# Optimization experiments

Measured on AMD Instinct MI355X. Metric: run time of the kernel, lower is better.

## Reference

```python
import jax, jax.numpy as jnp
import numpy as np

N, E, IN, HID, HEADS, L = 50000, 640000, 32, 64, 2, 4
MAXR = 8
N_ETYPE = 11 + 3 * MAXR  # 35
NEG_SLOPE = 0.2  # DGL EGATConv leaky_relu slope


def _mlp2(x, W1, b1, W2, b2):
    # 2-layer MLP: activation (gelu) after hidden layer only
    return jax.nn.gelu(x @ W1 + b1) @ W2 + b2


def _egat(h, ef, src, dst, W_ni, W_nj, W_fij, W_node, b_node, attn):
    # DGL EGATConv: edge-feature-enhanced graph attention
    n = h.shape[0]
    H, D = attn.shape
    f_edge = (h @ W_ni)[src] + (h @ W_nj)[dst] + ef @ W_fij       # [E, H*D]
    f_out = jax.nn.leaky_relu(f_edge, NEG_SLOPE).reshape(-1, H, D)
    e = jnp.einsum('ehd,hd->eh', f_out, attn)                     # [E, H]
    m = jax.ops.segment_max(e, dst, num_segments=n)               # per-dst max
    w = jnp.exp(e - m[dst])
    z = jax.ops.segment_sum(w, dst, num_segments=n)
    a = w / z[dst]                                                # edge softmax over incoming edges
    h_out = (h @ W_node + b_node).reshape(n, H, D)
    return jax.ops.segment_sum(h_out[src] * a[:, :, None], dst, num_segments=n)  # [N, H, D]


def _forward(feat, att_rc, att_rp, type_emb, rid_emb, rc_W, rc_b, rp_W, rp_b,
             fe_W1, fe_b1, fe_W2, fe_b2, W_ni, W_nj, W_fij, W_node, b_node, attn,
             mlp_W1, mlp_b1, mlp_W2, mlp_b2, src, dst, etype, erid):
    n = feat.shape[0]
    # edge embedding, 'sum' flavor
    ef = type_emb[etype] + rid_emb[erid] + att_rc @ rc_W + rc_b + att_rp @ rp_W + rp_b
    feats = [feat]
    h = _mlp2(feat, fe_W1, fe_b1, fe_W2, fe_b2)
    feats.append(h)
    for l in range(W_ni.shape[0]):
        agg = _egat(h, ef, src, dst, W_ni[l], W_nj[l], W_fij[l],
                    W_node[l], b_node[l], attn[l])
        h = _mlp2(agg.reshape(n, -1), mlp_W1[l], mlp_b1[l], mlp_W2[l], mlp_b2[l]) + h  # residual
        feats.append(h)
    node_emb = jnp.concatenate(feats, axis=-1)             # layer_pooling='all'
    graph_emb = jnp.max(node_emb, axis=0, keepdims=True)   # graph max pooling
    return jnp.concatenate([node_emb, jnp.broadcast_to(graph_emb, node_emb.shape)], axis=-1)


def setup_inputs() -> dict:
    key = jax.random.key(0)
    ks = iter(jax.random.split(key, 40))
    s = 0.05
    return {
        'feat': jax.random.normal(next(ks), (N, IN), jnp.float32),
        'att_rc': jax.random.normal(next(ks), (E, 2), jnp.float32),
        'att_rp': jax.random.normal(next(ks), (E, 3), jnp.float32),
        'type_emb': jax.random.normal(next(ks), (N_ETYPE, HID), jnp.float32) * s,
        'rid_emb': jax.random.normal(next(ks), (MAXR + 1, HID), jnp.float32) * s,
        'rc_W': jax.random.normal(next(ks), (2, HID), jnp.float32) * s,
        'rc_b': jnp.zeros((HID,), jnp.float32),
        'rp_W': jax.random.normal(next(ks), (3, HID), jnp.float32) * s,
        'rp_b': jnp.zeros((HID,), jnp.float32),
        'fe_W1': jax.random.normal(next(ks), (IN, HID), jnp.float32) * s,
        'fe_b1': jnp.zeros((HID,), jnp.float32),
        'fe_W2': jax.random.normal(next(ks), (HID, HID), jnp.float32) * s,
        'fe_b2': jnp.zeros((HID,), jnp.float32),
        'W_ni': jax.random.normal(next(ks), (L, HID, HEADS * HID), jnp.float32) * s,
        'W_nj': jax.random.normal(next(ks), (L, HID, HEADS * HID), jnp.float32) * s,
        'W_fij': jax.random.normal(next(ks), (L, HID, HEADS * HID), jnp.float32) * s,
        'W_node': jax.random.normal(next(ks), (L, HID, HEADS * HID), jnp.float32) * s,
        'b_node': jnp.zeros((L, HEADS * HID), jnp.float32),
        'attn': jax.random.normal(next(ks), (L, HEADS, HID), jnp.float32) * s,
        'mlp_W1': jax.random.normal(next(ks), (L, HEADS * HID, HEADS * HID), jnp.float32) * s,
        'mlp_b1': jnp.zeros((L, HEADS * HID), jnp.float32),
        'mlp_W2': jax.random.normal(next(ks), (L, HEADS * HID, HID), jnp.float32) * s,
        'mlp_b2': jnp.zeros((L, HID), jnp.float32),
        'src': jax.random.randint(next(ks), (E,), 0, N, jnp.int32),
        'dst': jax.random.randint(next(ks), (E,), 0, N, jnp.int32),
        'etype': jax.random.randint(next(ks), (E,), 0, N_ETYPE, jnp.int32),
        'erid': jax.random.randint(next(ks), (E,), 0, MAXR + 1, jnp.int32),
    }


def reference(feat, att_rc, att_rp, type_emb, rid_emb, rc_W, rc_b, rp_W, rp_b,
              fe_W1, fe_b1, fe_W2, fe_b2, W_ni, W_nj, W_fij, W_node, b_node, attn,
              mlp_W1, mlp_b1, mlp_W2, mlp_b2, src, dst, etype, erid):
    return _forward(feat, att_rc, att_rp, type_emb, rid_emb, rc_W, rc_b, rp_W, rp_b,
                    fe_W1, fe_b1, fe_W2, fe_b2, W_ni, W_nj, W_fij, W_node, b_node, attn,
                    mlp_W1, mlp_b1, mlp_W2, mlp_b2, src, dst, etype, erid)
```

## Files before the change

### kernel.cpp

```cpp
#include <hip/hip_runtime.h>
#include <math.h>

#define N_NODES 50000
#define N_EDGES 640000
#define NLAYER  4
#define NPAD    50016

typedef unsigned short bf16_t;
typedef __attribute__((ext_vector_type(8))) short s16x8;
typedef __attribute__((ext_vector_type(4))) float f32x4;

__device__ __forceinline__ float gelu_f(float x) {
    return 0.5f * x * (1.0f + tanhf(0.7978845608028654f * (x + 0.044715f * x * x * x)));
}

__device__ __forceinline__ bf16_t f2bf(float f) {
    unsigned u = __float_as_uint(f);
    unsigned r = (u + 0x7FFFu + ((u >> 16) & 1u)) >> 16;
    return (bf16_t)r;
}
__device__ __forceinline__ float bf2f(bf16_t h) { return __uint_as_float(((unsigned)h) << 16); }
__device__ __forceinline__ float bfl(unsigned x) { return __uint_as_float(x << 16); }
__device__ __forceinline__ float bfh(unsigned x) { return __uint_as_float(x & 0xFFFF0000u); }

__global__ void k_zero32(unsigned* p, int n) {
    int i = blockIdx.x * 256 + threadIdx.x;
    if (i < n) p[i] = 0u;
}

__global__ void k_hist(const int* __restrict__ dst, int* __restrict__ deg) {
    int i = blockIdx.x * 256 + threadIdx.x;
    if (i < N_EDGES) atomicAdd(&deg[dst[i]], 1);
}

__global__ void k_scan1(const int* __restrict__ deg, int* __restrict__ rowptr, int* __restrict__ bsum) {
    __shared__ int sd[1024];
    int gi = blockIdx.x * 1024 + threadIdx.x;
    int v = (gi < N_NODES) ? deg[gi] : 0;
    sd[threadIdx.x] = v;
    __syncthreads();
    for (int off = 1; off < 1024; off <<= 1) {
        int t2 = (threadIdx.x >= (unsigned)off) ? sd[threadIdx.x - off] : 0;
        __syncthreads();
        sd[threadIdx.x] += t2;
        __syncthreads();
    }
    if (gi < N_NODES) rowptr[gi] = sd[threadIdx.x] - v;
    if (threadIdx.x == 1023) bsum[blockIdx.x] = sd[1023];
}

__global__ void k_scan2(const int* __restrict__ bsum, int* __restrict__ boff, int nb) {
    if (threadIdx.x == 0 && blockIdx.x == 0) {
        int run = 0;
        for (int b = 0; b < nb; b++) { boff[b] = run; run += bsum[b]; }
    }
}

__global__ void k_scan3(int* __restrict__ rowptr, const int* __restrict__ boff) {
    int gi = blockIdx.x * 1024 + threadIdx.x;
    if (gi < N_NODES) rowptr[gi] += boff[blockIdx.x];
    if (gi == 0) rowptr[N_NODES] = N_EDGES;
}

__global__ void k_copy(const int* __restrict__ a, int* __restrict__ b) {
    int i = blockIdx.x * 256 + threadIdx.x;
    if (i < N_NODES) b[i] = a[i];
}

__global__ void k_scatter(const int* __restrict__ dst, int* __restrict__ cursor, int* __restrict__ eidx) {
    int i = blockIdx.x * 256 + threadIdx.x;
    if (i < N_EDGES) {
        int p = atomicAdd(&cursor[dst[i]], 1);
        eidx[p] = i;
    }
}

__global__ void k_sortgather(
    const int* __restrict__ eidx, const int* __restrict__ src, const int* __restrict__ dst,
    const int* __restrict__ etype, const int* __restrict__ erid,
    const float* __restrict__ att_rc, const float* __restrict__ att_rp,
    int* __restrict__ src_s, uint4* __restrict__ emA, uint2* __restrict__ emB)
{
    int i = blockIdx.x * 256 + threadIdx.x;
    if (i < N_EDGES) {
        int e = eidx[i];
        int sv = src[e];
        src_s[i] = sv;
        uint4 a;
        a.x = (unsigned)sv;
        a.y = (unsigned)dst[e];
        a.z = (unsigned)(etype[e] * 9 + erid[e]);
        a.w = (unsigned)f2bf(att_rc[2 * e]) | ((unsigned)f2bf(att_rc[2 * e + 1]) << 16);
        uint2 b;
        b.x = (unsigned)f2bf(att_rp[3 * e]) | ((unsigned)f2bf(att_rp[3 * e + 1]) << 16);
        b.y = (unsigned)f2bf(att_rp[3 * e + 2]);
        emA[i] = a;
        emB[i] = b;
    }
}

__global__ void k_base(const float* __restrict__ type_emb, const float* __restrict__ rid_emb,
                       const float* __restrict__ rcb, const float* __restrict__ rpb,
                       float* __restrict__ base)
{
    int idx = blockIdx.x * 256 + threadIdx.x;
    if (idx >= 315 * 64) return;
    int c = idx >> 6, k = idx & 63;
    int et = c / 9, er = c % 9;
    base[idx] = type_emb[et * 64 + k] + rid_emb[er * 64 + k] + rcb[k] + rpb[k];
}

__global__ void k_wprep(const float* __restrict__ Wfij, const float* __restrict__ Wni,
                        const float* __restrict__ Wnj, const float* __restrict__ Wnode,
                        const float* __restrict__ W1, const float* __restrict__ W2,
                        bf16_t* __restrict__ WT, bf16_t* __restrict__ W3T,
                        bf16_t* __restrict__ W1T, bf16_t* __restrict__ W2T)
{
    int idx = blockIdx.x * 256 + threadIdx.x;
    if (idx >= NLAYER * 57344) return;
    int l = idx / 57344, r = idx % 57344;
    if (r < 8192) {
        int n = r >> 6, k = r & 63;
        WT[l * 8192 + r] = f2bf(Wfij[l * 8192 + k * 128 + n]);
    } else if (r < 32768) {
        int q = r - 8192; int c = q >> 6, k = q & 63;
        const float* src = (c < 128) ? Wni : (c < 256) ? Wnj : Wnode;
        W3T[l * 24576 + q] = f2bf(src[l * 8192 + k * 128 + (c & 127)]);
    } else if (r < 49152) {
        int q = r - 32768; int n = q >> 7, k = q & 127;
        W1T[l * 16384 + q] = f2bf(W1[l * 16384 + k * 128 + n]);
    } else {
        int q = r - 49152; int j = q >> 7, k = q & 127;
        W2T[l * 8192 + q] = f2bf(W2[l * 8192 + k * 64 + j]);
    }
}

__global__ __launch_bounds__(256) void k_fe(
    const float* __restrict__ feat, const float* __restrict__ W1, const float* __restrict__ b1,
    const float* __restrict__ W2, const float* __restrict__ b2,
    float* __restrict__ h, bf16_t* __restrict__ hb, float* __restrict__ out)
{
    __shared__ float hid[4][64];
    int w = threadIdx.x >> 6, lane = threadIdx.x & 63;
    int n = blockIdx.x * 4 + w;
    float a = b1[lane];
#pragma unroll 8
    for (int k = 0; k < 32; k++) a = fmaf(feat[n * 32 + k], W1[k * 64 + lane], a);
    hid[w][lane] = gelu_f(a);
    __syncthreads();
    float o = b2[lane];
#pragma unroll 8
    for (int k = 0; k < 64; k++) o = fmaf(hid[w][k], W2[k * 64 + lane], o);
    h[n * 64 + lane] = o;
    hb[n * 64 + lane] = f2bf(o);
    out[n * 704 + 32 + lane] = o;
    if (lane < 32) out[n * 704 + lane] = feat[n * 32 + lane];
}

__global__ __launch_bounds__(256) void k_node3(
    const bf16_t* __restrict__ hb, const bf16_t* __restrict__ W3T,
    const float* __restrict__ bnode, bf16_t* __restrict__ s)
{
    __shared__ __align__(16) bf16_t hbS[32 * 72];
    const int t = threadIdx.x;
    const int wave = t >> 6, lane = t & 63, l16 = lane & 15, quad = lane >> 4;
    const int n0 = blockIdx.x * 32;
    {
        int r = t >> 3, sg = t & 7;
        *(s16x8*)(hbS + r * 72 + sg * 8) = *(const s16x8*)(hb + (size_t)(n0 + r) * 64 + sg * 8);
    }
    __syncthreads();
    const int ng = wave & 1, ch = wave >> 1;
    const s16x8 B0 = *(const s16x8*)(hbS + (ng * 16 + l16) * 72 + quad * 8);
    const s16x8 B1 = *(const s16x8*)(hbS + (ng * 16 + l16) * 72 + 32 + quad * 8);
    const int node = n0 + ng * 16 + l16;
#pragma unroll
    for (int nt = 0; nt < 12; nt++) {
        int c0 = ch * 192 + nt * 16;
        const s16x8 A0 = *(const s16x8*)(W3T + (size_t)(c0 + l16) * 64 + quad * 8);
        const s16x8 A1 = *(const s16x8*)(W3T + (size_t)(c0 + l16) * 64 + 32 + quad * 8);
        f32x4 acc = {0.f, 0.f, 0.f, 0.f};
        acc = __builtin_amdgcn_mfma_f32_16x16x32_bf16(A0, B0, acc, 0, 0, 0);
        acc = __builtin_amdgcn_mfma_f32_16x16x32_bf16(A1, B1, acc, 0, 0, 0);
        int cb = c0 + quad * 4;
        float4 bv = make_float4(0.f, 0.f, 0.f, 0.f);
        if (cb >= 256) bv = *(const float4*)(bnode + cb - 256);
        ushort4 o;
        o.x = f2bf(acc[0] + bv.x);
        o.y = f2bf(acc[1] + bv.y);
        o.z = f2bf(acc[2] + bv.z);
        o.w = f2bf(acc[3] + bv.w);
        *(ushort4*)(s + (size_t)node * 384 + cb) = o;
    }
}

__global__ __launch_bounds__(256) void k_edge(
    const bf16_t* __restrict__ s, const bf16_t* __restrict__ WT,
    const float* __restrict__ attn, const uint4* __restrict__ emA,
    const uint2* __restrict__ emB, const float* __restrict__ base,
    const float* __restrict__ rcW, const float* __restrict__ rpW,
    float* __restrict__ evals)
{
    const int lane = threadIdx.x & 63;
    const int l16 = lane & 15, quad = lane >> 4;
    const int unit = (blockIdx.x * 256 + threadIdx.x) >> 6;
    const int iA = unit * 32 + l16, iB = iA + 16;

    const uint4 mA = emA[iA], mB = emA[iB];
    const uint2 nA = emB[iA], nB = emB[iB];

    ushort4 nivA[4], njvA[4], nivB[4], njvB[4];
    {
        const bf16_t* srA = s + (size_t)mA.x * 384;
        const bf16_t* drA = s + (size_t)mA.y * 384 + 128;
        const bf16_t* srB = s + (size_t)mB.x * 384;
        const bf16_t* drB = s + (size_t)mB.y * 384 + 128;
#pragma unroll
        for (int mt = 0; mt < 4; mt++) {
            const int d0 = mt * 16 + quad * 4;
            nivA[mt] = *(const ushort4*)(srA + d0);
            njvA[mt] = *(const ushort4*)(drA + d0);
            nivB[mt] = *(const ushort4*)(srB + d0);
            njvB[mt] = *(const ushort4*)(drB + d0);
        }
    }

    const float rcA0 = bfl(mA.w), rcA1 = bfh(mA.w);
    const float rpA0 = bfl(nA.x), rpA1 = bfh(nA.x), rpA2 = bfl(nA.y);
    const float rcB0 = bfl(mB.w), rcB1 = bfh(mB.w);
    const float rpB0 = bfl(nB.x), rpB1 = bfh(nB.x), rpB2 = bfl(nB.y);
    const float* bpA = base + (size_t)mA.z * 64;
    const float* bpB = base + (size_t)mB.z * 64;

    s16x8 B0A, B1A, B0B, B1B;
#pragma unroll
    for (int s4 = 0; s4 < 4; s4++) {
        const int k = (s4 >> 1) * 32 + (s4 & 1) * 4 + quad * 8;
        const float4 w0 = *(const float4*)(rcW + k);
        const float4 w1 = *(const float4*)(rcW + 64 + k);
        const float4 w2 = *(const float4*)(rpW + k);
        const float4 w3 = *(const float4*)(rpW + 64 + k);
        const float4 w4 = *(const float4*)(rpW + 128 + k);
        const float4 bA = *(const float4*)(bpA + k);
        const float4 bB = *(const float4*)(bpB + k);
        float a0 = bA.x, a1 = bA.y, a2 = bA.z, a3 = bA.w;
        a0 = fmaf(rcA0, w0.x, a0); a1 = fmaf(rcA0, w0.y, a1); a2 = fmaf(rcA0, w0.z, a2); a3 = fmaf(rcA0, w0.w, a3);
        a0 = fmaf(rcA1, w1.x, a0); a1 = fmaf(rcA1, w1.y, a1); a2 = fmaf(rcA1, w1.z, a2); a3 = fmaf(rcA1, w1.w, a3);
        a0 = fmaf(rpA0, w2.x, a0); a1 = fmaf(rpA0, w2.y, a1); a2 = fmaf(rpA0, w2.z, a2); a3 = fmaf(rpA0, w2.w, a3);
        a0 = fmaf(rpA1, w3.x, a0); a1 = fmaf(rpA1, w3.y, a1); a2 = fmaf(rpA1, w3.z, a2); a3 = fmaf(rpA1, w3.w, a3);
        a0 = fmaf(rpA2, w4.x, a0); a1 = fmaf(rpA2, w4.y, a1); a2 = fmaf(rpA2, w4.z, a2); a3 = fmaf(rpA2, w4.w, a3);
        float b0 = bB.x, b1 = bB.y, b2 = bB.z, b3 = bB.w;
        b0 = fmaf(rcB0, w0.x, b0); b1 = fmaf(rcB0, w0.y, b1); b2 = fmaf(rcB0, w0.z, b2); b3 = fmaf(rcB0, w0.w, b3);
        b0 = fmaf(rcB1, w1.x, b0); b1 = fmaf(rcB1, w1.y, b1); b2 = fmaf(rcB1, w1.z, b2); b3 = fmaf(rcB1, w1.w, b3);
        b0 = fmaf(rpB0, w2.x, b0); b1 = fmaf(rpB0, w2.y, b1); b2 = fmaf(rpB0, w2.z, b2); b3 = fmaf(rpB0, w2.w, b3);
        b0 = fmaf(rpB1, w3.x, b0); b1 = fmaf(rpB1, w3.y, b1); b2 = fmaf(rpB1, w3.z, b2); b3 = fmaf(rpB1, w3.w, b3);
        b0 = fmaf(rpB2, w4.x, b0); b1 = fmaf(rpB2, w4.y, b1); b2 = fmaf(rpB2, w4.z, b2); b3 = fmaf(rpB2, w4.w, b3);
        const short pA0 = (short)f2bf(a0), pA1 = (short)f2bf(a1), pA2 = (short)f2bf(a2), pA3 = (short)f2bf(a3);
        const short pB0 = (short)f2bf(b0), pB1 = (short)f2bf(b1), pB2 = (short)f2bf(b2), pB3 = (short)f2bf(b3);
        const int o = (s4 & 1) * 4;
        if (s4 < 2) {
            B0A[o + 0] = pA0; B0A[o + 1] = pA1; B0A[o + 2] = pA2; B0A[o + 3] = pA3;
            B0B[o + 0] = pB0; B0B[o + 1] = pB1; B0B[o + 2] = pB2; B0B[o + 3] = pB3;
        } else {
            B1A[o + 0] = pA0; B1A[o + 1] = pA1; B1A[o + 2] = pA2; B1A[o + 3] = pA3;
            B1B[o + 0] = pB0; B1B[o + 1] = pB1; B1B[o + 2] = pB2; B1B[o + 3] = pB3;
        }
    }

    float sndA[4][4], sndB[4][4];
#pragma unroll
    for (int mt = 0; mt < 4; mt++) {
        sndA[mt][0] = bf2f(nivA[mt].x) + bf2f(njvA[mt].x);
        sndA[mt][1] = bf2f(nivA[mt].y) + bf2f(njvA[mt].y);
        sndA[mt][2] = bf2f(nivA[mt].z) + bf2f(njvA[mt].z);
        sndA[mt][3] = bf2f(nivA[mt].w) + bf2f(njvA[mt].w);
        sndB[mt][0] = bf2f(nivB[mt].x) + bf2f(njvB[mt].x);
        sndB[mt][1] = bf2f(nivB[mt].y) + bf2f(njvB[mt].y);
        sndB[mt][2] = bf2f(nivB[mt].z) + bf2f(njvB[mt].z);
        sndB[mt][3] = bf2f(nivB[mt].w) + bf2f(njvB[mt].w);
    }

#pragma unroll
    for (int hd = 0; hd < 2; hd++) {
        float pA = 0.f, pB = 0.f;
#pragma unroll
        for (int mt = 0; mt < 4; mt++) {
            const bf16_t* arow = WT + (hd * 64 + mt * 16 + l16) * 64 + quad * 8;
            const s16x8 A0 = *(const s16x8*)(arow);
            const s16x8 A1 = *(const s16x8*)(arow + 32);
            f32x4 aA = {0.f, 0.f, 0.f, 0.f};
            aA = __builtin_amdgcn_mfma_f32_16x16x32_bf16(A0, B0A, aA, 0, 0, 0);
            aA = __builtin_amdgcn_mfma_f32_16x16x32_bf16(A1, B1A, aA, 0, 0, 0);
            f32x4 aB = {0.f, 0.f, 0.f, 0.f};
            aB = __builtin_amdgcn_mfma_f32_16x16x32_bf16(A0, B0B, aB, 0, 0, 0);
            aB = __builtin_amdgcn_mfma_f32_16x16x32_bf16(A1, B1B, aB, 0, 0, 0);
            const float4 at = *(const float4*)(attn + hd * 64 + mt * 16 + quad * 4);
            float f0 = aA[0] + sndA[mt][0];
            float f1 = aA[1] + sndA[mt][1];
            float f2 = aA[2] + sndA[mt][2];
            float f3 = aA[3] + sndA[mt][3];
            f0 = (f0 >= 0.f) ? f0 : 0.2f * f0;
            f1 = (f1 >= 0.f) ? f1 : 0.2f * f1;
            f2 = (f2 >= 0.f) ? f2 : 0.2f * f2;
            f3 = (f3 >= 0.f) ? f3 : 0.2f * f3;
            pA = fmaf(f0, at.x, pA);
            pA = fmaf(f1, at.y, pA);
            pA = fmaf(f2, at.z, pA);
            pA = fmaf(f3, at.w, pA);
            float g0 = aB[0] + sndB[mt][0];
            float g1 = aB[1] + sndB[mt][1];
            float g2 = aB[2] + sndB[mt][2];
            float g3 = aB[3] + sndB[mt][3];
            g0 = (g0 >= 0.f) ? g0 : 0.2f * g0;
            g1 = (g1 >= 0.f) ? g1 : 0.2f * g1;
            g2 = (g2 >= 0.f) ? g2 : 0.2f * g2;
            g3 = (g3 >= 0.f) ? g3 : 0.2f * g3;
            pB = fmaf(g0, at.x, pB);
            pB = fmaf(g1, at.y, pB);
            pB = fmaf(g2, at.z, pB);
            pB = fmaf(g3, at.w, pB);
        }
        pA += __shfl_xor(pA, 16);
        pA += __shfl_xor(pA, 32);
        pB += __shfl_xor(pB, 16);
        pB += __shfl_xor(pB, 32);
        if (quad == 0) {
            evals[iA * 2 + hd] = pA;
            evals[iB * 2 + hd] = pB;
        }
    }
}

__global__ __launch_bounds__(256) void k_soft_agg(
    const int* __restrict__ rowptr, const int* __restrict__ src_s,
    const float* __restrict__ evals, const bf16_t* __restrict__ s,
    unsigned* __restrict__ aggb)
{
    int lane = threadIdx.x & 63;
    int wid = (blockIdx.x * 256 + threadIdx.x) >> 6;
    int nw = (gridDim.x * 256) >> 6;
    const int hb = (lane >> 4) & 1;
    const int esel = lane >> 5;
    const int s32 = (lane & 15) | ((lane >> 5) << 4);
    const int dsel = (lane & 31) * 4;
    for (int n = wid; n < N_NODES; n += nw) {
        int r0 = rowptr[n], r1 = rowptr[n + 1];
        if (r0 == r1) {
            if (lane < 32) { uint2 z; z.x = 0u; z.y = 0u; *(uint2*)(aggb + (size_t)n * 64 + lane * 2) = z; }
            continue;
        }
        float mm = -1e30f;
        for (int i = r0 + s32; i < r1; i += 32) mm = fmaxf(mm, evals[2 * i + hb]);
        mm = fmaxf(mm, __shfl_xor(mm, 1));
        mm = fmaxf(mm, __shfl_xor(mm, 2));
        mm = fmaxf(mm, __shfl_xor(mm, 4));
        mm = fmaxf(mm, __shfl_xor(mm, 8));
        mm = fmaxf(mm, __shfl_xor(mm, 32));
        float z = 0.f;
        for (int i = r0 + s32; i < r1; i += 32) z += expf(evals[2 * i + hb] - mm);
        z += __shfl_xor(z, 1);
        z += __shfl_xor(z, 2);
        z += __shfl_xor(z, 4);
        z += __shfl_xor(z, 8);
        z += __shfl_xor(z, 32);
        float rz = 1.f / z;
        float acc0 = 0.f, acc1 = 0.f, acc2 = 0.f, acc3 = 0.f;
        for (int i = r0; i < r1; i += 8) {
            uint2 cc[4]; float ww[4];
#pragma unroll
            for (int p = 0; p < 4; p++) {
                int ej = i + 2 * p + esel;
                bool v = ej < r1;
                int es = v ? ej : r0;
                cc[p] = *(const uint2*)(s + (size_t)src_s[es] * 384 + 256 + dsel);
                ww[p] = v ? expf(evals[2 * ej + hb] - mm) * rz : 0.f;
            }
#pragma unroll
            for (int p = 0; p < 4; p++) {
                acc0 = fmaf(ww[p], bfl(cc[p].x), acc0);
                acc1 = fmaf(ww[p], bfh(cc[p].x), acc1);
                acc2 = fmaf(ww[p], bfl(cc[p].y), acc2);
                acc3 = fmaf(ww[p], bfh(cc[p].y), acc3);
            }
        }
        acc0 += __shfl_xor(acc0, 32);
        acc1 += __shfl_xor(acc1, 32);
        acc2 += __shfl_xor(acc2, 32);
        acc3 += __shfl_xor(acc3, 32);
        if (lane < 32) {
            uint2 o;
            o.x = (unsigned)f2bf(acc0) | ((unsigned)f2bf(acc1) << 16);
            o.y = (unsigned)f2bf(acc2) | ((unsigned)f2bf(acc3) << 16);
            *(uint2*)(aggb + (size_t)n * 64 + lane * 2) = o;
        }
    }
}

__global__ __launch_bounds__(256) void k_mlp(
    const bf16_t* __restrict__ aggb, const bf16_t* __restrict__ W1T, const float* __restrict__ b1,
    const bf16_t* __restrict__ W2T, const float* __restrict__ b2,
    const float* __restrict__ hin, float* __restrict__ hout, bf16_t* __restrict__ houtb,
    float* __restrict__ out, int col0)
{
    __shared__ __align__(16) bf16_t aggS[32 * 136];
    __shared__ __align__(16) bf16_t hidS[32 * 136];
    const int t = threadIdx.x;
    const int wave = t >> 6, lane = t & 63, l16 = lane & 15, quad = lane >> 4;
    const int n0 = blockIdx.x * 32;
    {
        int r = t >> 3, sg = t & 7;
        *(s16x8*)(aggS + r * 136 + sg * 16) =
            *(const s16x8*)(aggb + (size_t)(n0 + r) * 128 + sg * 16);
        *(s16x8*)(aggS + r * 136 + sg * 16 + 8) =
            *(const s16x8*)(aggb + (size_t)(n0 + r) * 128 + sg * 16 + 8);
    }
    __syncthreads();
    const int ng = wave & 1, nh = wave >> 1;
    const int node = n0 + ng * 16 + l16;
    {
        const bf16_t* brow = aggS + (ng * 16 + l16) * 136 + quad * 8;
        s16x8 B[4];
#pragma unroll
        for (int ks = 0; ks < 4; ks++) B[ks] = *(const s16x8*)(brow + ks * 32);
#pragma unroll
        for (int nt = 0; nt < 4; nt++) {
            int nb = nh * 64 + nt * 16;
            f32x4 acc = {0.f, 0.f, 0.f, 0.f};
#pragma unroll
            for (int ks = 0; ks < 4; ks++) {
                const s16x8 A = *(const s16x8*)(W1T + (size_t)(nb + l16) * 128 + ks * 32 + quad * 8);
                acc = __builtin_amdgcn_mfma_f32_16x16x32_bf16(A, B[ks], acc, 0, 0, 0);
            }
            const float4 bv = *(const float4*)(b1 + nb + quad * 4);
            ushort4 o;
            o.x = f2bf(gelu_f(acc[0] + bv.x));
            o.y = f2bf(gelu_f(acc[1] + bv.y));
            o.z = f2bf(gelu_f(acc[2] + bv.z));
            o.w = f2bf(gelu_f(acc[3] + bv.w));
            *(ushort4*)(hidS + (ng * 16 + l16) * 136 + nb + quad * 4) = o;
        }
    }
    __syncthreads();
    {
        const int jh = wave >> 1;
        const bf16_t* hrow = hidS + (ng * 16 + l16) * 136 + quad * 8;
        s16x8 H[4];
#pragma unroll
        for (int ks = 0; ks < 4; ks++) H[ks] = *(const s16x8*)(hrow + ks * 32);
#pragma unroll
        for (int jt = 0; jt < 2; jt++) {
            int jb = jh * 32 + jt * 16;
            f32x4 acc = {0.f, 0.f, 0.f, 0.f};
#pragma unroll
            for (int ks = 0; ks < 4; ks++) {
                const s16x8 A = *(const s16x8*)(W2T + (size_t)(jb + l16) * 128 + ks * 32 + quad * 8);
                acc = __builtin_amdgcn_mfma_f32_16x16x32_bf16(A, H[ks], acc, 0, 0, 0);
            }
            int j0 = jb + quad * 4;
            const float4 bv = *(const float4*)(b2 + j0);
            const float4 hv = *(const float4*)(hin + (size_t)node * 64 + j0);
            float4 v;
            v.x = acc[0] + bv.x + hv.x;
            v.y = acc[1] + bv.y + hv.y;
            v.z = acc[2] + bv.z + hv.z;
            v.w = acc[3] + bv.w + hv.w;
            *(float4*)(hout + (size_t)node * 64 + j0) = v;
            ushort4 ob;
            ob.x = f2bf(v.x); ob.y = f2bf(v.y); ob.z = f2bf(v.z); ob.w = f2bf(v.w);
            *(ushort4*)(houtb + (size_t)node * 64 + j0) = ob;
            if (node < N_NODES)
                *(float4*)(out + (size_t)node * 704 + col0 + j0) = v;
        }
    }
}

__device__ __forceinline__ unsigned fmap(float v) {
    unsigned u = __float_as_uint(v);
    return (u & 0x80000000u) ? ~u : (u | 0x80000000u);
}

__global__ __launch_bounds__(384) void k_colmax(const float* __restrict__ out, unsigned* __restrict__ gmax) {
    int c = threadIdx.x;
    if (c >= 352) return;
    float m = -1e30f;
    for (int n = blockIdx.x; n < N_NODES; n += gridDim.x)
        m = fmaxf(m, out[(size_t)n * 704 + c]);
    atomicMax(gmax + c, fmap(m));
}

__global__ __launch_bounds__(384) void k_bcast(const unsigned* __restrict__ gmax, float* __restrict__ out) {
    int c = threadIdx.x;
    if (c >= 352) return;
    unsigned u = gmax[c];
    u = (u & 0x80000000u) ? (u ^ 0x80000000u) : ~u;
    float v = __uint_as_float(u);
    for (int n = blockIdx.x; n < N_NODES; n += gridDim.x)
        out[(size_t)n * 704 + 352 + c] = v;
}

extern "C" void kernel_launch(void* const* d_in, const int* in_sizes, int n_in,
                              void* d_out, int out_size, void* d_ws, size_t ws_size,
                              hipStream_t stream)
{
    (void)in_sizes; (void)n_in; (void)out_size; (void)ws_size;
    const float* feat     = (const float*)d_in[0];
    const float* att_rc   = (const float*)d_in[1];
    const float* att_rp   = (const float*)d_in[2];
    const float* type_emb = (const float*)d_in[3];
    const float* rid_emb  = (const float*)d_in[4];
    const float* rc_W     = (const float*)d_in[5];
    const float* rc_b     = (const float*)d_in[6];
    const float* rp_W     = (const float*)d_in[7];
    const float* rp_b     = (const float*)d_in[8];
    const float* fe_W1    = (const float*)d_in[9];
    const float* fe_b1    = (const float*)d_in[10];
    const float* fe_W2    = (const float*)d_in[11];
    const float* fe_b2    = (const float*)d_in[12];
    const float* W_ni     = (const float*)d_in[13];
    const float* W_nj     = (const float*)d_in[14];
    const float* W_fij    = (const float*)d_in[15];
    const float* W_node   = (const float*)d_in[16];
    const float* b_node   = (const float*)d_in[17];
    const float* attn     = (const float*)d_in[18];
    const float* mlp_W1   = (const float*)d_in[19];
    const float* mlp_b1   = (const float*)d_in[20];
    const float* mlp_W2   = (const float*)d_in[21];
    const float* mlp_b2   = (const float*)d_in[22];
    const int* src   = (const int*)d_in[23];
    const int* dst   = (const int*)d_in[24];
    const int* etype = (const int*)d_in[25];
    const int* erid  = (const int*)d_in[26];
    float* out = (float*)d_out;

    char* cur = (char*)d_ws;
    auto alloc = [&](size_t bytes) { char* p = cur; cur += (bytes + 15) & ~(size_t)15; return p; };
    float* h_a    = (float*)alloc((size_t)NPAD * 64 * 4);
    float* h_b    = (float*)alloc((size_t)NPAD * 64 * 4);
    bf16_t* hb_a  = (bf16_t*)alloc((size_t)NPAD * 64 * 2);
    bf16_t* hb_b  = (bf16_t*)alloc((size_t)NPAD * 64 * 2);
    bf16_t* s     = (bf16_t*)alloc((size_t)NPAD * 384 * 2);
    float* ev     = (float*)alloc((size_t)N_EDGES * 2 * 4);
    bf16_t* aggb  = (bf16_t*)alloc((size_t)NPAD * 128 * 2);
    int* deg     = (int*)alloc((size_t)N_NODES * 4);
    int* rowptr  = (int*)alloc((size_t)(N_NODES + 1) * 4);
    int* cursor  = (int*)alloc((size_t)N_NODES * 4);
    int* eidx    = (int*)alloc((size_t)N_EDGES * 4);
    int* src_s   = (int*)alloc((size_t)N_EDGES * 4);
    uint4* emA   = (uint4*)alloc((size_t)N_EDGES * 16);
    uint2* emB   = (uint2*)alloc((size_t)N_EDGES * 8);
    float* baseT = (float*)alloc((size_t)315 * 64 * 4);
    bf16_t* WT   = (bf16_t*)alloc((size_t)NLAYER * 128 * 64 * 2);
    bf16_t* W3T  = (bf16_t*)alloc((size_t)NLAYER * 384 * 64 * 2);
    bf16_t* W1T  = (bf16_t*)alloc((size_t)NLAYER * 128 * 128 * 2);
    bf16_t* W2T  = (bf16_t*)alloc((size_t)NLAYER * 64 * 128 * 2);
    int* bsum    = (int*)alloc(64 * 4);
    int* boff    = (int*)alloc(64 * 4);
    unsigned* gmax = (unsigned*)alloc(352 * 4);

    const int NB = (N_NODES + 1023) / 1024;

    k_zero32<<<(N_NODES + 255) / 256, 256, 0, stream>>>((unsigned*)deg, N_NODES);
    k_zero32<<<2, 256, 0, stream>>>(gmax, 352);
    k_hist<<<N_EDGES / 256, 256, 0, stream>>>(dst, deg);
    k_scan1<<<NB, 1024, 0, stream>>>(deg, rowptr, bsum);
    k_scan2<<<1, 64, 0, stream>>>(bsum, boff, NB);
    k_scan3<<<NB, 1024, 0, stream>>>(rowptr, boff);
    k_copy<<<(N_NODES + 255) / 256, 256, 0, stream>>>(rowptr, cursor);
    k_scatter<<<N_EDGES / 256, 256, 0, stream>>>(dst, cursor, eidx);
    k_sortgather<<<N_EDGES / 256, 256, 0, stream>>>(eidx, src, dst, etype, erid, att_rc, att_rp,
                                                    src_s, emA, emB);
    k_base<<<(315 * 64 + 255) / 256, 256, 0, stream>>>(type_emb, rid_emb, rc_b, rp_b, baseT);
    k_wprep<<<(NLAYER * 57344 + 255) / 256, 256, 0, stream>>>(
        W_fij, W_ni, W_nj, W_node, mlp_W1, mlp_W2, WT, W3T, W1T, W2T);
    k_fe<<<N_NODES / 4, 256, 0, stream>>>(feat, fe_W1, fe_b1, fe_W2, fe_b2, h_a, hb_a, out);

    float* hc = h_a;  bf16_t* hbc = hb_a;
    float* hn = h_b;  bf16_t* hbn = hb_b;
    for (int l = 0; l < NLAYER; l++) {
        k_node3<<<NPAD / 32, 256, 0, stream>>>(hbc, W3T + (size_t)l * 384 * 64, b_node + l * 128, s);
        k_edge<<<N_EDGES / 128, 256, 0, stream>>>(s, WT + l * 128 * 64, attn + l * 128,
                                                  emA, emB, baseT, rc_W, rp_W, ev);
        k_soft_agg<<<4096, 256, 0, stream>>>(rowptr, src_s, ev, s, (unsigned*)aggb);
        k_mlp<<<NPAD / 32, 256, 0, stream>>>(aggb, W1T + (size_t)l * 128 * 128, mlp_b1 + l * 128,
                                             W2T + (size_t)l * 64 * 128, mlp_b2 + l * 64,
                                             hc, hn, hbn, out, 32 + 64 * (l + 1));
        float* tf = hc; hc = hn; hn = tf;
        bf16_t* tb = hbc; hbc = hbn; hbn = tb;
    }
    k_colmax<<<512, 384, 0, stream>>>(out, gmax);
    k_bcast<<<512, 384, 0, stream>>>(gmax, out);
}
```

Baseline: 1.264 ms.

## Make edge-score kernel persistent with prefetched gathers and LDS-staged weights

Replaces the one-shot edge kernel with a persistent grid where each wave processes 10 tiles of 16 edges. The next tile's metadata and gathered node rows are prefetched while the current tile is computed. The per-layer edge-projection weights, attention vector and rc/rp weights are staged once per block into shared memory in an MFMA-friendly lane order. The aim is to hide gather latency and cut repeated global weight loads, at the cost of fewer in-flight edges per wave and a fixed grid size tied to the edge count.

```diff
diff --git a/kernel.cpp b/kernel.cpp
--- a/kernel.cpp
+++ b/kernel.cpp
@@ -5,6 +5,9 @@
 #define N_EDGES 640000
 #define NLAYER  4
 #define NPAD    50016
+
+#define EDGE_BLOCKS 1000
+#define EDGE_WAVES  4000
 
 typedef unsigned short bf16_t;
 typedef __attribute__((ext_vector_type(8))) short s16x8;
@@ -194,6 +197,80 @@
     }
 }
 
+__device__ __forceinline__ void eg_issue(
+    const bf16_t* __restrict__ s, const uint4& ma, int quad, ushort4 (&G)[8])
+{
+    const bf16_t* sr = s + (size_t)ma.x * 384;
+    const bf16_t* dr = s + (size_t)ma.y * 384 + 128;
+#pragma unroll
+    for (int mt = 0; mt < 4; mt++) {
+        const int d0 = mt * 16 + quad * 4;
+        G[mt]     = *(const ushort4*)(sr + d0);
+        G[4 + mt] = *(const ushort4*)(dr + d0);
+    }
+}
+
+__device__ __forceinline__ void eg_process(
+    int i, const uint4& ma, const uint2& mb, const ushort4 (&G)[8],
+    const bf16_t* __restrict__ WTs, const float* __restrict__ attL,
+    const float (*__restrict__ cwL)[64], const float* __restrict__ base,
+    int lane, int quad, float* __restrict__ evals)
+{
+    const float rc0 = bfl(ma.w), rc1 = bfh(ma.w);
+    const float rp0 = bfl(mb.x), rp1 = bfh(mb.x), rp2 = bfl(mb.y);
+    const float* bp = base + (size_t)ma.z * 64;
+    s16x8 B0, B1;
+#pragma unroll
+    for (int s4 = 0; s4 < 4; s4++) {
+        const int k = (s4 >> 1) * 32 + (s4 & 1) * 4 + quad * 8;
+        const float4 bv = *(const float4*)(bp + k);
+        const float4 w0 = *(const float4*)(&cwL[0][k]);
+        const float4 w1 = *(const float4*)(&cwL[1][k]);
+        const float4 w2 = *(const float4*)(&cwL[2][k]);
+        const float4 w3 = *(const float4*)(&cwL[3][k]);
+        const float4 w4 = *(const float4*)(&cwL[4][k]);
+        float v0 = bv.x, v1 = bv.y, v2 = bv.z, v3 = bv.w;
+        v0 = fmaf(rc0, w0.x, v0); v1 = fmaf(rc0, w0.y, v1); v2 = fmaf(rc0, w0.z, v2); v3 = fmaf(rc0, w0.w, v3);
+        v0 = fmaf(rc1, w1.x, v0); v1 = fmaf(rc1, w1.y, v1); v2 = fmaf(rc1, w1.z, v2); v3 = fmaf(rc1, w1.w, v3);
+        v0 = fmaf(rp0, w2.x, v0); v1 = fmaf(rp0, w2.y, v1); v2 = fmaf(rp0, w2.z, v2); v3 = fmaf(rp0, w2.w, v3);
+        v0 = fmaf(rp1, w3.x, v0); v1 = fmaf(rp1, w3.y, v1); v2 = fmaf(rp1, w3.z, v2); v3 = fmaf(rp1, w3.w, v3);
+        v0 = fmaf(rp2, w4.x, v0); v1 = fmaf(rp2, w4.y, v1); v2 = fmaf(rp2, w4.z, v2); v3 = fmaf(rp2, w4.w, v3);
+        const short p0 = (short)f2bf(v0), p1 = (short)f2bf(v1), p2 = (short)f2bf(v2), p3 = (short)f2bf(v3);
+        const int o = (s4 & 1) * 4;
+        if (s4 < 2) { B0[o] = p0; B0[o + 1] = p1; B0[o + 2] = p2; B0[o + 3] = p3; }
+        else        { B1[o] = p0; B1[o + 1] = p1; B1[o + 2] = p2; B1[o + 3] = p3; }
+    }
+#pragma unroll
+    for (int hd = 0; hd < 2; hd++) {
+        float p = 0.f;
+#pragma unroll
+        for (int mt = 0; mt < 4; mt++) {
+            const int fm = hd * 4 + mt;
+            const s16x8 A0 = *(const s16x8*)(WTs + ((fm * 2 + 0) * 64 + lane) * 8);
+            const s16x8 A1 = *(const s16x8*)(WTs + ((fm * 2 + 1) * 64 + lane) * 8);
+            f32x4 a = {0.f, 0.f, 0.f, 0.f};
+            a = __builtin_amdgcn_mfma_f32_16x16x32_bf16(A0, B0, a, 0, 0, 0);
+            a = __builtin_amdgcn_mfma_f32_16x16x32_bf16(A1, B1, a, 0, 0, 0);
+            const float4 at = *(const float4*)(attL + hd * 64 + mt * 16 + quad * 4);
+            float f0 = a[0] + (bf2f(G[mt].x) + bf2f(G[4 + mt].x));
+            float f1 = a[1] + (bf2f(G[mt].y) + bf2f(G[4 + mt].y));
+            float f2 = a[2] + (bf2f(G[mt].z) + bf2f(G[4 + mt].z));
+            float f3 = a[3] + (bf2f(G[mt].w) + bf2f(G[4 + mt].w));
+            f0 = (f0 >= 0.f) ? f0 : 0.2f * f0;
+            f1 = (f1 >= 0.f) ? f1 : 0.2f * f1;
+            f2 = (f2 >= 0.f) ? f2 : 0.2f * f2;
+            f3 = (f3 >= 0.f) ? f3 : 0.2f * f3;
+            p = fmaf(f0, at.x, p);
+            p = fmaf(f1, at.y, p);
+            p = fmaf(f2, at.z, p);
+            p = fmaf(f3, at.w, p);
+        }
+        p += __shfl_xor(p, 16);
+        p += __shfl_xor(p, 32);
+        if (quad == 0) evals[i * 2 + hd] = p;
+    }
+}
+
 __global__ __launch_bounds__(256) void k_edge(
     const bf16_t* __restrict__ s, const bf16_t* __restrict__ WT,
     const float* __restrict__ attn, const uint4* __restrict__ emA,
@@ -201,133 +278,55 @@
     const float* __restrict__ rcW, const float* __restrict__ rpW,
     float* __restrict__ evals)
 {
+    __shared__ __align__(16) bf16_t WTs[16 * 64 * 8];
+    __shared__ __align__(16) float attL[128];
+    __shared__ __align__(16) float cwL[5][64];
+    for (int c = threadIdx.x; c < 1024; c += 256) {
+        int ln = c & 63, rowq = c >> 6;
+        int half = rowq & 1, fm = rowq >> 1;
+        int rl16 = ln & 15, rq = ln >> 4;
+        int grow = (fm >> 2) * 64 + (fm & 3) * 16 + rl16;
+        *(s16x8*)(WTs + c * 8) = *(const s16x8*)(WT + grow * 64 + half * 32 + rq * 8);
+    }
+    if (threadIdx.x < 128) attL[threadIdx.x] = attn[threadIdx.x];
+    {
+        int j = threadIdx.x >> 6, k = threadIdx.x & 63;
+        cwL[j][k] = (j < 2) ? rcW[j * 64 + k] : rpW[(j - 2) * 64 + k];
+        if (threadIdx.x < 64) cwL[4][threadIdx.x] = rpW[128 + threadIdx.x];
+    }
+    __syncthreads();
+
     const int lane = threadIdx.x & 63;
     const int l16 = lane & 15, quad = lane >> 4;
-    const int unit = (blockIdx.x * 256 + threadIdx.x) >> 6;
-    const int iA = unit * 32 + l16, iB = iA + 16;
-
-    const uint4 mA = emA[iA], mB = emA[iB];
-    const uint2 nA = emB[iA], nB = emB[iB];
-
-    ushort4 nivA[4], njvA[4], nivB[4], njvB[4];
-    {
-        const bf16_t* srA = s + (size_t)mA.x * 384;
-        const bf16_t* drA = s + (size_t)mA.y * 384 + 128;
-        const bf16_t* srB = s + (size_t)mB.x * 384;
-        const bf16_t* drB = s + (size_t)mB.y * 384 + 128;
-#pragma unroll
-        for (int mt = 0; mt < 4; mt++) {
-            const int d0 = mt * 16 + quad * 4;
-            nivA[mt] = *(const ushort4*)(srA + d0);
-            njvA[mt] = *(const ushort4*)(drA + d0);
-            nivB[mt] = *(const ushort4*)(srB + d0);
-            njvB[mt] = *(const ushort4*)(drB + d0);
-        }
-    }
-
-    const float rcA0 = bfl(mA.w), rcA1 = bfh(mA.w);
-    const float rpA0 = bfl(nA.x), rpA1 = bfh(nA.x), rpA2 = bfl(nA.y);
-    const float rcB0 = bfl(mB.w), rcB1 = bfh(mB.w);
-    const float rpB0 = bfl(nB.x), rpB1 = bfh(nB.x), rpB2 = bfl(nB.y);
-    const float* bpA = base + (size_t)mA.z * 64;
-    const float* bpB = base + (size_t)mB.z * 64;
-
-    s16x8 B0A, B1A, B0B, B1B;
-#pragma unroll
-    for (int s4 = 0; s4 < 4; s4++) {
-        const int k = (s4 >> 1) * 32 + (s4 & 1) * 4 + quad * 8;
-        const float4 w0 = *(const float4*)(rcW + k);
-        const float4 w1 = *(const float4*)(rcW + 64 + k);
-        const float4 w2 = *(const float4*)(rpW + k);
-        const float4 w3 = *(const float4*)(rpW + 64 + k);
-        const float4 w4 = *(const float4*)(rpW + 128 + k);
-        const float4 bA = *(const float4*)(bpA + k);
-        const float4 bB = *(const float4*)(bpB + k);
-        float a0 = bA.x, a1 = bA.y, a2 = bA.z, a3 = bA.w;
-        a0 = fmaf(rcA0, w0.x, a0); a1 = fmaf(rcA0, w0.y, a1); a2 = fmaf(rcA0, w0.z, a2); a3 = fmaf(rcA0, w0.w, a3);
-        a0 = fmaf(rcA1, w1.x, a0); a1 = fmaf(rcA1, w1.y, a1); a2 = fmaf(rcA1, w1.z, a2); a3 = fmaf(rcA1, w1.w, a3);
-        a0 = fmaf(rpA0, w2.x, a0); a1 = fmaf(rpA0, w2.y, a1); a2 = fmaf(rpA0, w2.z, a2); a3 = fmaf(rpA0, w2.w, a3);
-        a0 = fmaf(rpA1, w3.x, a0); a1 = fmaf(rpA1, w3.y, a1); a2 = fmaf(rpA1, w3.z, a2); a3 = fmaf(rpA1, w3.w, a3);
-        a0 = fmaf(rpA2, w4.x, a0); a1 = fmaf(rpA2, w4.y, a1); a2 = fmaf(rpA2, w4.z, a2); a3 = fmaf(rpA2, w4.w, a3);
-        float b0 = bB.x, b1 = bB.y, b2 = bB.z, b3 = bB.w;
-        b0 = fmaf(rcB0, w0.x, b0); b1 = fmaf(rcB0, w0.y, b1); b2 = fmaf(rcB0, w0.z, b2); b3 = fmaf(rcB0, w0.w, b3);
-        b0 = fmaf(rcB1, w1.x, b0); b1 = fmaf(rcB1, w1.y, b1); b2 = fmaf(rcB1, w1.z, b2); b3 = fmaf(rcB1, w1.w, b3);
-        b0 = fmaf(rpB0, w2.x, b0); b1 = fmaf(rpB0, w2.y, b1); b2 = fmaf(rpB0, w2.z, b2); b3 = fmaf(rpB0, w2.w, b3);
-        b0 = fmaf(rpB1, w3.x, b0); b1 = fmaf(rpB1, w3.y, b1); b2 = fmaf(rpB1, w3.z, b2); b3 = fmaf(rpB1, w3.w, b3);
-        b0 = fmaf(rpB2, w4.x, b0); b1 = fmaf(rpB2, w4.y, b1); b2 = fmaf(rpB2, w4.z, b2); b3 = fmaf(rpB2, w4.w, b3);
-        const short pA0 = (short)f2bf(a0), pA1 = (short)f2bf(a1), pA2 = (short)f2bf(a2), pA3 = (short)f2bf(a3);
-        const short pB0 = (short)f2bf(b0), pB1 = (short)f2bf(b1), pB2 = (short)f2bf(b2), pB3 = (short)f2bf(b3);
-        const int o = (s4 & 1) * 4;
-        if (s4 < 2) {
-            B0A[o + 0] = pA0; B0A[o + 1] = pA1; B0A[o + 2] = pA2; B0A[o + 3] = pA3;
-            B0B[o + 0] = pB0; B0B[o + 1] = pB1; B0B[o + 2] = pB2; B0B[o + 3] = pB3;
-        } else {
-            B1A[o + 0] = pA0; B1A[o + 1] = pA1; B1A[o + 2] = pA2; B1A[o + 3] = pA3;
-            B1B[o + 0] = pB0; B1B[o + 1] = pB1; B1B[o + 2] = pB2; B1B[o + 3] = pB3;
-        }
-    }
-
-    float sndA[4][4], sndB[4][4];
-#pragma unroll
-    for (int mt = 0; mt < 4; mt++) {
-        sndA[mt][0] = bf2f(nivA[mt].x) + bf2f(njvA[mt].x);
-        sndA[mt][1] = bf2f(nivA[mt].y) + bf2f(njvA[mt].y);
-        sndA[mt][2] = bf2f(nivA[mt].z) + bf2f(njvA[mt].z);
-        sndA[mt][3] = bf2f(nivA[mt].w) + bf2f(njvA[mt].w);
-        sndB[mt][0] = bf2f(nivB[mt].x) + bf2f(njvB[mt].x);
-        sndB[mt][1] = bf2f(nivB[mt].y) + bf2f(njvB[mt].y);
-        sndB[mt][2] = bf2f(nivB[mt].z) + bf2f(njvB[mt].z);
-        sndB[mt][3] = bf2f(nivB[mt].w) + bf2f(njvB[mt].w);
-    }
-
-#pragma unroll
-    for (int hd = 0; hd < 2; hd++) {
-        float pA = 0.f, pB = 0.f;
-#pragma unroll
-        for (int mt = 0; mt < 4; mt++) {
-            const bf16_t* arow = WT + (hd * 64 + mt * 16 + l16) * 64 + quad * 8;
-            const s16x8 A0 = *(const s16x8*)(arow);
-            const s16x8 A1 = *(const s16x8*)(arow + 32);
-            f32x4 aA = {0.f, 0.f, 0.f, 0.f};
-            aA = __builtin_amdgcn_mfma_f32_16x16x32_bf16(A0, B0A, aA, 0, 0, 0);
-            aA = __builtin_amdgcn_mfma_f32_16x16x32_bf16(A1, B1A, aA, 0, 0, 0);
-            f32x4 aB = {0.f, 0.f, 0.f, 0.f};
-            aB = __builtin_amdgcn_mfma_f32_16x16x32_bf16(A0, B0B, aB, 0, 0, 0);
-            aB = __builtin_amdgcn_mfma_f32_16x16x32_bf16(A1, B1B, aB, 0, 0, 0);
-            const float4 at = *(const float4*)(attn + hd * 64 + mt * 16 + quad * 4);
-            float f0 = aA[0] + sndA[mt][0];
-            float f1 = aA[1] + sndA[mt][1];
-            float f2 = aA[2] + sndA[mt][2];
-            float f3 = aA[3] + sndA[mt][3];
-            f0 = (f0 >= 0.f) ? f0 : 0.2f * f0;
-            f1 = (f1 >= 0.f) ? f1 : 0.2f * f1;
-            f2 = (f2 >= 0.f) ? f2 : 0.2f * f2;
-            f3 = (f3 >= 0.f) ? f3 : 0.2f * f3;
-            pA = fmaf(f0, at.x, pA);
-            pA = fmaf(f1, at.y, pA);
-            pA = fmaf(f2, at.z, pA);
-            pA = fmaf(f3, at.w, pA);
-            float g0 = aB[0] + sndB[mt][0];
-            float g1 = aB[1] + sndB[mt][1];
-            float g2 = aB[2] + sndB[mt][2];
-            float g3 = aB[3] + sndB[mt][3];
-            g0 = (g0 >= 0.f) ? g0 : 0.2f * g0;
-            g1 = (g1 >= 0.f) ? g1 : 0.2f * g1;
-            g2 = (g2 >= 0.f) ? g2 : 0.2f * g2;
-            g3 = (g3 >= 0.f) ? g3 : 0.2f * g3;
-            pB = fmaf(g0, at.x, pB);
-            pB = fmaf(g1, at.y, pB);
-            pB = fmaf(g2, at.z, pB);
-            pB = fmaf(g3, at.w, pB);
-        }
-        pA += __shfl_xor(pA, 16);
-        pA += __shfl_xor(pA, 32);
-        pB += __shfl_xor(pB, 16);
-        pB += __shfl_xor(pB, 32);
-        if (quad == 0) {
-            evals[iA * 2 + hd] = pA;
-            evals[iB * 2 + hd] = pB;
-        }
+    const int wid = (blockIdx.x * 256 + threadIdx.x) >> 6;
+
+    ushort4 GA[8], GB[8];
+    uint4 maC = emA[wid * 16 + l16];
+    uint2 mbC = emB[wid * 16 + l16];
+    eg_issue(s, maC, quad, GA);
+    uint4 maN = emA[(wid + EDGE_WAVES) * 16 + l16];
+    uint2 mbN = emB[(wid + EDGE_WAVES) * 16 + l16];
+
+#pragma unroll 1
+    for (int it = 0; it < 5; it++) {
+        const int ta = wid + (2 * it) * EDGE_WAVES;
+        const int tb = ta + EDGE_WAVES;
+        eg_issue(s, maN, quad, GB);
+        const bool h = it < 4;
+        uint4 ma2 = maC; uint2 mb2 = mbC;
+        if (h) {
+            int e2 = (tb + EDGE_WAVES) * 16 + l16;
+            ma2 = emA[e2]; mb2 = emB[e2];
+        }
+        eg_process(ta * 16 + l16, maC, mbC, GA, WTs, attL, cwL, base, lane, quad, evals);
+        if (h) eg_issue(s, ma2, quad, GA);
+        uint4 ma3 = maN; uint2 mb3 = mbN;
+        if (h) {
+            int e3 = (tb + 2 * EDGE_WAVES) * 16 + l16;
+            ma3 = emA[e3]; mb3 = emB[e3];
+        }
+        eg_process(tb * 16 + l16, maN, mbN, GB, WTs, attL, cwL, base, lane, quad, evals);
+        maC = ma2; mbC = mb2; maN = ma3; mbN = mb3;
     }
 }
 
@@ -578,8 +577,8 @@
     float* hn = h_b;  bf16_t* hbn = hb_b;
     for (int l = 0; l < NLAYER; l++) {
         k_node3<<<NPAD / 32, 256, 0, stream>>>(hbc, W3T + (size_t)l * 384 * 64, b_node + l * 128, s);
-        k_edge<<<N_EDGES / 128, 256, 0, stream>>>(s, WT + l * 128 * 64, attn + l * 128,
-                                                  emA, emB, baseT, rc_W, rp_W, ev);
+        k_edge<<<EDGE_BLOCKS, 256, 0, stream>>>(s, WT + l * 128 * 64, attn + l * 128,
+                                                emA, emB, baseT, rc_W, rp_W, ev);
         k_soft_agg<<<4096, 256, 0, stream>>>(rowptr, src_s, ev, s, (unsigned*)aggb);
         k_mlp<<<NPAD / 32, 256, 0, stream>>>(aggb, W1T + (size_t)l * 128 * 128, mlp_b1 + l * 128,
                                              W2T + (size_t)l * 64 * 128, mlp_b2 + l * 64,
```

Measured after the change: 1.258 ms. About the same (-0.5%).
